# Kernel tuning notes

Measured on AMD Instinct MI355X. Metric: run time of the kernel, lower is better.

The kernel has to match this reference:

```python
import jax, jax.numpy as jnp
import numpy as np

NF, D, H = 32, 256, 128  # n_features, d_model, d_model//2
B, T = 16, 512
EPS = 1e-5

def _ln(x, g, b):
    m = jnp.mean(x, axis=-1, keepdims=True)
    v = jnp.mean((x - m) ** 2, axis=-1, keepdims=True)
    return (x - m) * jax.lax.rsqrt(v + EPS) * g + b


def setup_inputs() -> dict:
    key = jax.random.key(0)
    ks = jax.random.split(key, 16)
    s = 0.05
    inp = {
        "x": jax.random.normal(ks[0], (B, T, NF), dtype=jnp.float32),
        # batched per-feature GRN params (d_in=1 -> fc1 weight is (NF,H))
        "w1": jax.random.normal(ks[1], (NF, H)) * s,
        "b1": jnp.zeros((NF, H)),
        "w2": jax.random.normal(ks[2], (NF, H, D)) * s,
        "b2": jnp.zeros((NF, D)),
        "wg": jax.random.normal(ks[3], (NF, H, D)) * s,
        "bg": jnp.zeros((NF, D)),
        "ws": jax.random.normal(ks[4], (NF, D)) * s,  # skip Linear(1,D)
        "bs": jnp.zeros((NF, D)),
        "ln_g": jnp.ones((NF, D)),
        "ln_b": jnp.zeros((NF, D)),
        # weight GRN: d_in=NF*D, d_hidden=D, d_out=NF
        "W1": jax.random.normal(ks[5], (NF * D, D)) * s,
        "B1": jnp.zeros((D,)),
        "W2": jax.random.normal(ks[6], (D, NF)) * s,
        "B2": jnp.zeros((NF,)),
        "Wg": jax.random.normal(ks[7], (D, NF)) * s,
        "Bg": jnp.zeros((NF,)),
        "Ws": jax.random.normal(ks[8], (NF * D, NF)) * s,
        "Bs": jnp.zeros((NF,)),
        "LN_g": jnp.ones((NF,)),
        "LN_b": jnp.zeros((NF,)),
    }
    return inp


def reference(x, w1, b1, w2, b2, wg, bg, ws, bs, ln_g, ln_b,
              W1, B1, W2, B2, Wg, Bg, Ws, Bs, LN_g, LN_b):
    Bn, Tn, Fn = x.shape
    # --- all per-feature GRNs batched over the feature axis (dropout=eval/identity) ---
    h = jax.nn.elu(x[..., None] * w1 + b1)                      # (B,T,F,H)
    proj = jnp.einsum('btfh,fhd->btfd', h, w2) + b2             # (B,T,F,D)
    gate = jax.nn.sigmoid(jnp.einsum('btfh,fhd->btfd', h, wg) + bg)
    skip = x[..., None] * ws + bs                               # (B,T,F,D)
    stacked = _ln(skip + gate * proj, ln_g, ln_b)               # (B,T,F,D)
    # --- softmax feature weights from mean-pooled flat features ---
    flat_pooled = stacked.mean(axis=1).reshape(Bn, Fn * stacked.shape[-1])  # (B,F*D)
    hw = jax.nn.elu(flat_pooled @ W1 + B1)                      # (B,D)
    pw = hw @ W2 + B2
    gw = jax.nn.sigmoid(hw @ Wg + Bg)
    wgrn = _ln(flat_pooled @ Ws + Bs + gw * pw, LN_g, LN_b)     # (B,F)
    weights = jax.nn.softmax(wgrn, axis=-1)                     # (B,F)
    # --- weighted feature combine ---
    selected = jnp.einsum('btfd,bf->btd', stacked, weights)     # (B,T,D)
    return selected, weights
```

## Files before the change

### kernel.cpp

```cpp
#include <hip/hip_runtime.h>
#include <hip/hip_fp16.h>

#define NF 32
#define DM 256
#define HH 128
#define BB 16
#define TT 512
#define BT 8192
#define OUT_W_OFF 2097152
#define EPS 1e-5f

typedef __bf16 bf16x8 __attribute__((ext_vector_type(8)));
typedef float  f32x16 __attribute__((ext_vector_type(16)));
typedef __fp16 f16x2 __attribute__((ext_vector_type(2)));
typedef __fp16 f16x8 __attribute__((ext_vector_type(8)));

__device__ __forceinline__ float eluf(float z){ return z > 0.f ? z : __expf(z) - 1.f; }
__device__ __forceinline__ float sigm(float z){ return 1.f/(1.f + __expf(-z)); }
__device__ __forceinline__ unsigned f2bf(float x){
  unsigned u = __float_as_uint(x);
  u += 0x7fffu + ((u>>16)&1u);
  return u>>16;
}

template<int MT, int NTHR>
__device__ __forceinline__ void build_A(uint4* Apack, const float* __restrict__ x,
                                        const float* __restrict__ w1, const float* __restrict__ b1,
                                        int f, int tok0, int tid){
  #pragma unroll
  for (int p = 0; p < (MT*512)/NTHR; ++p){
    int slot = tid + p*NTHR;
    int l  = slot & 63;
    int ks = (slot>>6)&7;
    int mt = slot>>9;
    int m  = mt*32 + (l&31);
    int k0 = ks*16 + (l>>5)*8;
    float xv = x[(tok0+m)*NF + f];
    const float* wp = w1 + f*HH + k0;
    const float* bp = b1 + f*HH + k0;
    float4 wa = *(const float4*)wp, wb = *(const float4*)(wp+4);
    float4 ba = *(const float4*)bp, bb = *(const float4*)(bp+4);
    bf16x8 v;
    v[0] = (__bf16)eluf(fmaf(xv, wa.x, ba.x));
    v[1] = (__bf16)eluf(fmaf(xv, wa.y, ba.y));
    v[2] = (__bf16)eluf(fmaf(xv, wa.z, ba.z));
    v[3] = (__bf16)eluf(fmaf(xv, wa.w, ba.w));
    v[4] = (__bf16)eluf(fmaf(xv, wb.x, bb.x));
    v[5] = (__bf16)eluf(fmaf(xv, wb.y, bb.y));
    v[6] = (__bf16)eluf(fmaf(xv, wb.z, bb.z));
    v[7] = (__bf16)eluf(fmaf(xv, wb.w, bb.w));
    Apack[slot] = __builtin_bit_cast(uint4, v);
  }
}

__global__ __launch_bounds__(256) void k_prep(const float* __restrict__ w2,
                                              const float* __restrict__ wgm,
                                              uint4* __restrict__ Wpk,
                                              float* __restrict__ pooled,
                                              float* __restrict__ hw_pre,
                                              float* __restrict__ sk_pre,
                                              unsigned* __restrict__ counter){
  __shared__ float ssrc[2][128][32];
  const int tid = threadIdx.x;
  const int f = blockIdx.x, c = blockIdx.y;
  {
    const int gb = blockIdx.y*gridDim.x + blockIdx.x;
    const int gt = gb*256 + tid;
    pooled[gt] = 0.f;
    pooled[gt + 65536] = 0.f;
    if (gt < 4096) hw_pre[gt] = 0.f;
    else if (gt < 4608) sk_pre[gt - 4096] = 0.f;
    if (gt == 0) *counter = 0u;
  }
  #pragma unroll
  for (int it = 0; it < 32; ++it){
    int idx = tid + it*256;
    int arr = idx >> 12;
    int rem = idx & 4095;
    int k = rem >> 5, dd = rem & 31;
    const float* src = arr ? wgm : w2;
    ssrc[arr][k][dd] = src[(f*HH + k)*DM + c*32 + dd];
  }
  __syncthreads();
  #pragma unroll
  for (int p = 0; p < 4; ++p){
    int oc = tid + p*256;
    int nt = oc>>9, ks = (oc>>6)&7, l = oc&63;
    int k0 = ks*16 + (l>>5)*8, dd = l&31;
    float v[8];
    #pragma unroll
    for (int j=0;j<8;++j) v[j] = ssrc[nt][k0+j][dd];
    uint4 pk;
    pk.x = f2bf(v[0]) | (f2bf(v[1])<<16);
    pk.y = f2bf(v[2]) | (f2bf(v[3])<<16);
    pk.z = f2bf(v[4]) | (f2bf(v[5])<<16);
    pk.w = f2bf(v[6]) | (f2bf(v[7])<<16);
    Wpk[(f*8 + c)*1024 + oc] = pk;
  }
}

__global__ __launch_bounds__(512, 2) void k_pass1(const float* __restrict__ x,  const float* __restrict__ w1,
    const float* __restrict__ b1, const float* __restrict__ b2, const float* __restrict__ bg,
    const float* __restrict__ wsk, const float* __restrict__ bsk,
    const float* __restrict__ lng, const float* __restrict__ lnb,
    const uint4* __restrict__ Wpk,
    float* __restrict__ pooled, uint4* __restrict__ stk4){
  __shared__ uint4 smem[4096];
  __shared__ float xs[128];
  __shared__ float poolbuf[256];
  const int tid = threadIdx.x, lane = tid&63, wid = tid>>6;
  const int tt = wid>>1, ch = wid&1;
  const int col = lane&31, q = lane>>5;
  const int f = blockIdx.y;
  const int tok0 = blockIdx.x*128;
  const int b = tok0 >> 9;
  if (tid < 256) poolbuf[tid] = 0.f;
  if (tid < 128) xs[tid] = x[(tok0 + tid)*NF + f];

  build_A<4,512>(smem, x, w1, b1, f, tok0, tid);
  __syncthreads();
  bf16x8 afr[8];
  #pragma unroll
  for (int ks=0; ks<8; ++ks) afr[ks] = __builtin_bit_cast(bf16x8, smem[(tt*8+ks)*64 + lane]);
  __syncthreads();

  __fp16* stage = (__fp16*)smem;
  #pragma unroll 1
  for (int ci=0; ci<4; ++ci){
    const int c = ch*4 + ci;
    const uint4* wb = Wpk + (f*8 + c)*1024;
    bf16x8 bfr[8];
    #pragma unroll
    for (int ks=0;ks<8;++ks) bfr[ks] = __builtin_bit_cast(bf16x8, wb[ks*64 + lane]);
    f32x16 acc0 = {0.f};
    #pragma unroll
    for (int ks=0;ks<8;++ks) acc0 = __builtin_amdgcn_mfma_f32_32x32x16_bf16(afr[ks], bfr[ks], acc0, 0,0,0);
    __builtin_amdgcn_sched_barrier(0);
    #pragma unroll
    for (int ks=0;ks<8;++ks) bfr[ks] = __builtin_bit_cast(bf16x8, wb[512 + ks*64 + lane]);
    f32x16 acc1 = {0.f};
    #pragma unroll
    for (int ks=0;ks<8;++ks) acc1 = __builtin_amdgcn_mfma_f32_32x32x16_bf16(afr[ks], bfr[ks], acc1, 0,0,0);
    __builtin_amdgcn_sched_barrier(0);
    const int d = c*32 + col;
    const float b2v = b2[f*DM+d], bgv = bg[f*DM+d];
    #pragma unroll
    for (int i=0;i<8;++i){
      const int r0 = 2*i, r1 = r0+1;
      const int t0 = tt*32 + (r0&3) + 8*(i>>1) + 4*q;
      stage[ t0   *256 + d] = (__fp16)(sigm(acc1[r0]+bgv)*(acc0[r0]+b2v));
      stage[(t0+1)*256 + d] = (__fp16)(sigm(acc1[r1]+bgv)*(acc0[r1]+b2v));
    }
  }
  __syncthreads();

  const int oc = tid & 31;
  float4 ga = *(const float4*)(lng + f*DM + oc*8);
  float4 gb = *(const float4*)(lng + f*DM + oc*8 + 4);
  float4 la = *(const float4*)(lnb + f*DM + oc*8);
  float4 lb = *(const float4*)(lnb + f*DM + oc*8 + 4);
  float4 wa = *(const float4*)(wsk + f*DM + oc*8);
  float4 wbv = *(const float4*)(wsk + f*DM + oc*8 + 4);
  float4 sa = *(const float4*)(bsk + f*DM + oc*8);
  float4 sb = *(const float4*)(bsk + f*DM + oc*8 + 4);
  float gj[8] = {ga.x,ga.y,ga.z,ga.w,gb.x,gb.y,gb.z,gb.w};
  float bj[8] = {la.x,la.y,la.z,la.w,lb.x,lb.y,lb.z,lb.w};
  float wj[8] = {wa.x,wa.y,wa.z,wa.w,wbv.x,wbv.y,wbv.z,wbv.w};
  float cj[8] = {sa.x,sa.y,sa.z,sa.w,sb.x,sb.y,sb.z,sb.w};
  float ps[8];
  #pragma unroll
  for (int j=0;j<8;++j) ps[j]=0.f;
  #pragma unroll
  for (int p=0;p<8;++p){
    int slot = tid + p*512;
    int t = slot >> 5;
    uint4 v = smem[slot];
    f16x8 s8 = __builtin_bit_cast(f16x8, v);
    float xt = xs[t];
    float s[8];
    float ssum = 0.f, ssq = 0.f;
    #pragma unroll
    for (int j=0;j<8;++j){
      s[j] = fmaf(xt, wj[j], cj[j]) + (float)s8[j];
      ssum += s[j];
      ssq = fmaf(s[j], s[j], ssq);
    }
    ssum += __shfl_xor(ssum,1);  ssq += __shfl_xor(ssq,1);
    ssum += __shfl_xor(ssum,2);  ssq += __shfl_xor(ssq,2);
    ssum += __shfl_xor(ssum,4);  ssq += __shfl_xor(ssq,4);
    ssum += __shfl_xor(ssum,8);  ssq += __shfl_xor(ssq,8);
    ssum += __shfl_xor(ssum,16); ssq += __shfl_xor(ssq,16);
    float mu = ssum * (1.f/256.f);
    float var = fmaf(-mu, mu, ssq*(1.f/256.f));
    float rs = rsqrtf(fmaxf(var, 0.f) + EPS);
    float nmr = -mu*rs;
    float sh[8];
    #pragma unroll
    for (int j=0;j<8;++j){
      sh[j] = fmaf(fmaf(s[j], rs, nmr), gj[j], bj[j]);
      ps[j] += sh[j];
    }
    uint4 pk;
    pk.x = __builtin_bit_cast(unsigned, __builtin_amdgcn_cvt_pkrtz(sh[0], sh[1]));
    pk.y = __builtin_bit_cast(unsigned, __builtin_amdgcn_cvt_pkrtz(sh[2], sh[3]));
    pk.z = __builtin_bit_cast(unsigned, __builtin_amdgcn_cvt_pkrtz(sh[4], sh[5]));
    pk.w = __builtin_bit_cast(unsigned, __builtin_amdgcn_cvt_pkrtz(sh[6], sh[7]));
    const int tg = tok0 + t;
    stk4[(size_t)(tg>>2)*4096 + (size_t)f*128 + (size_t)(tg&3)*32 + oc] = pk;
  }
  #pragma unroll
  for (int j=0;j<8;++j) ps[j] += __shfl_xor(ps[j], 32);
  if (q == 0){
    #pragma unroll
    for (int j=0;j<8;++j) atomicAdd(&poolbuf[oc*8 + j], ps[j]);
  }
  __syncthreads();
  if (tid < 256) atomicAdd(&pooled[b*8192 + f*DM + tid], poolbuf[tid]);
}

__global__ __launch_bounds__(256) void k_pass2(const float* __restrict__ pooled,
    const float* __restrict__ W1, const float* __restrict__ Wsm,
    float* __restrict__ hw_pre, float* __restrict__ sk_pre,
    const float* __restrict__ B1, const float* __restrict__ W2, const float* __restrict__ B2,
    const float* __restrict__ Wg, const float* __restrict__ Bg, const float* __restrict__ Bs,
    const float* __restrict__ LNg, const float* __restrict__ LNb,
    unsigned* __restrict__ counter, float* __restrict__ out, float* __restrict__ wsel){
  __shared__ float fl[512];
  __shared__ float hwt[16][256];
  __shared__ int amLast;
  const int tid = threadIdx.x;
  const int b = blockIdx.x;
  const int k0 = blockIdx.y * 512;
  fl[tid]       = pooled[b*8192 + k0 + tid]       * (1.f/512.f);
  fl[tid+256]   = pooled[b*8192 + k0 + tid + 256] * (1.f/512.f);
  __syncthreads();
  float acc = 0.f;
  const float* wcol = W1 + (size_t)k0*DM + tid;
  #pragma unroll 4
  for (int i=0;i<512;++i) acc = fmaf(fl[i], wcol[(size_t)i*DM], acc);
  atomicAdd(&hw_pre[b*DM + tid], acc);
  const int colj = tid & 31, sub = tid >> 5;
  float acc2 = 0.f;
  const float* wscol = Wsm + (size_t)(k0 + sub*64)*NF + colj;
  const float* fls = fl + sub*64;
  #pragma unroll 4
  for (int i=0;i<64;++i) acc2 = fmaf(fls[i], wscol[(size_t)i*NF], acc2);
  atomicAdd(&sk_pre[b*NF + colj], acc2);

  __threadfence();
  __syncthreads();
  if (tid == 0){
    unsigned old = atomicAdd(counter, 1u);
    amLast = (old == 255u) ? 1 : 0;
  }
  __syncthreads();
  if (!amLast) return;
  #pragma unroll
  for (int p=0;p<16;++p){
    float v = atomicAdd(&hw_pre[p*DM + tid], 0.f);
    hwt[p][tid] = eluf(v + B1[tid]);
  }
  __syncthreads();
  const int j = tid & 31;
  const int bl = tid >> 5;
  #pragma unroll 1
  for (int pass=0; pass<2; ++pass){
    const int bb = bl + pass*8;
    float ap = B2[j], ag = Bg[j];
    #pragma unroll 4
    for (int i=0;i<256;++i){ float h = hwt[bb][i]; ap = fmaf(h, W2[i*NF+j], ap); ag = fmaf(h, Wg[i*NF+j], ag); }
    float gw = sigm(ag);
    float v = atomicAdd(&sk_pre[bb*NF + j], 0.f) + Bs[j] + gw*ap;
    float s1 = v;
    s1 += __shfl_xor(s1,1); s1 += __shfl_xor(s1,2); s1 += __shfl_xor(s1,4); s1 += __shfl_xor(s1,8); s1 += __shfl_xor(s1,16);
    float mean = s1*(1.f/32.f);
    float dv = v - mean;
    float s2 = dv*dv;
    s2 += __shfl_xor(s2,1); s2 += __shfl_xor(s2,2); s2 += __shfl_xor(s2,4); s2 += __shfl_xor(s2,8); s2 += __shfl_xor(s2,16);
    float wn = fmaf(dv * rsqrtf(s2*(1.f/32.f) + EPS), LNg[j], LNb[j]);
    float mx = wn;
    mx = fmaxf(mx, __shfl_xor(mx,1)); mx = fmaxf(mx, __shfl_xor(mx,2)); mx = fmaxf(mx, __shfl_xor(mx,4));
    mx = fmaxf(mx, __shfl_xor(mx,8)); mx = fmaxf(mx, __shfl_xor(mx,16));
    float e = __expf(wn - mx);
    float se = e;
    se += __shfl_xor(se,1); se += __shfl_xor(se,2); se += __shfl_xor(se,4); se += __shfl_xor(se,8); se += __shfl_xor(se,16);
    float wgt = e / se;
    out[OUT_W_OFF + bb*NF + j] = wgt;
    wsel[bb*NF + j] = wgt;
  }
}

__global__ __launch_bounds__(256) void k_comb(const uint4* __restrict__ stk4,
    const float* __restrict__ wsel, float* __restrict__ out){
  __shared__ float wloc[NF];
  const int tid = threadIdx.x, lane = tid&63;
  const int tc = blockIdx.x;
  const int ts = tid>>6;
  const int t = tc*4 + ts;
  const int b = t >> 9;
  if (tid < NF) wloc[tid] = wsel[b*NF + tid];
  __syncthreads();
  const int oc = lane&31, fh = lane>>5;
  float acc[8];
  #pragma unroll
  for (int j=0;j<8;++j) acc[j]=0.f;
  #pragma unroll
  for (int j=0;j<16;++j){
    int f = fh*16 + j;
    uint4 v = stk4[(size_t)tc*4096 + f*128 + ts*32 + oc];
    f16x8 hv = __builtin_bit_cast(f16x8, v);
    float wf = wloc[f];
    #pragma unroll
    for (int jj=0;jj<8;++jj) acc[jj] = fmaf(wf, (float)hv[jj], acc[jj]);
  }
  #pragma unroll
  for (int jj=0;jj<8;++jj) acc[jj] += __shfl_xor(acc[jj], 32);
  if (fh == 0){
    float4* o = (float4*)(out + (size_t)t*DM + oc*8);
    o[0] = make_float4(acc[0],acc[1],acc[2],acc[3]);
    o[1] = make_float4(acc[4],acc[5],acc[6],acc[7]);
  }
}

extern "C" void kernel_launch(void* const* d_in, const int* in_sizes, int n_in,
                              void* d_out, int out_size, void* d_ws, size_t ws_size,
                              hipStream_t stream) {
  const float* x   = (const float*)d_in[0];
  const float* w1  = (const float*)d_in[1];
  const float* b1  = (const float*)d_in[2];
  const float* w2  = (const float*)d_in[3];
  const float* b2  = (const float*)d_in[4];
  const float* wgm = (const float*)d_in[5];
  const float* bg  = (const float*)d_in[6];
  const float* wsk = (const float*)d_in[7];
  const float* bsk = (const float*)d_in[8];
  const float* lng = (const float*)d_in[9];
  const float* lnb = (const float*)d_in[10];
  const float* W1  = (const float*)d_in[11];
  const float* B1  = (const float*)d_in[12];
  const float* W2  = (const float*)d_in[13];
  const float* B2  = (const float*)d_in[14];
  const float* Wg  = (const float*)d_in[15];
  const float* Bg  = (const float*)d_in[16];
  const float* Wsm = (const float*)d_in[17];
  const float* Bs  = (const float*)d_in[18];
  const float* LNg = (const float*)d_in[19];
  const float* LNb = (const float*)d_in[20];
  float* out = (float*)d_out;

  char* ws = (char*)d_ws;
  uint4* Wpk      = (uint4*)ws;
  uint4* stk4     = (uint4*)(ws + 4194304);
  float* pooled   = (float*)(ws + 138412032);
  float* hw_pre   = (float*)(ws + 138936320);
  float* sk_pre   = (float*)(ws + 138952704);
  float* wsel     = (float*)(ws + 138954752);
  unsigned* cnt   = (unsigned*)(ws + 138956800);

  k_prep<<<dim3(32,8), 256, 0, stream>>>(w2, wgm, Wpk, pooled, hw_pre, sk_pre, cnt);
  k_pass1<<<dim3(64,32), 512, 0, stream>>>(x, w1, b1, b2, bg, wsk, bsk, lng, lnb,
                                           Wpk, pooled, stk4);
  k_pass2<<<dim3(16,16), 256, 0, stream>>>(pooled, W1, Wsm, hw_pre, sk_pre,
                                           B1, W2, B2, Wg, Bg, Bs, LNg, LNb,
                                           cnt, out, wsel);
  k_comb<<<2048, 256, 0, stream>>>(stk4, wsel, out);
}
```

Baseline: 325.7 us.

## Batch all 16 rows per W1 load in pass2 GEMV to reuse weights

The pass2 reduction is reorganized so that each block handles a 64-row slice of W1 for all 16 batch rows at once, instead of one batch row per block. Each W1 element is read once and reused across 16 accumulators, which cuts W1 global traffic by 16x. The grid shrinks from 256 blocks to 128, with the last-block counter threshold adjusted to match. In exchange the kernel has fewer blocks, more registers per thread, and more atomics per block.

After: 292.8 us. 1.11x faster.

```diff
diff --git a/kernel.cpp b/kernel.cpp
--- a/kernel.cpp
+++ b/kernel.cpp
@@ -225,33 +225,46 @@
     const float* __restrict__ Wg, const float* __restrict__ Bg, const float* __restrict__ Bs,
     const float* __restrict__ LNg, const float* __restrict__ LNb,
     unsigned* __restrict__ counter, float* __restrict__ out, float* __restrict__ wsel){
-  __shared__ float fl[512];
+  __shared__ float fl[16][64];
   __shared__ float hwt[16][256];
   __shared__ int amLast;
   const int tid = threadIdx.x;
-  const int b = blockIdx.x;
-  const int k0 = blockIdx.y * 512;
-  fl[tid]       = pooled[b*8192 + k0 + tid]       * (1.f/512.f);
-  fl[tid+256]   = pooled[b*8192 + k0 + tid + 256] * (1.f/512.f);
-  __syncthreads();
-  float acc = 0.f;
-  const float* wcol = W1 + (size_t)k0*DM + tid;
+  const int k0 = blockIdx.x * 64;
+  #pragma unroll
+  for (int p=0;p<4;++p){
+    int idx = tid + p*256;
+    int bb = idx >> 6, ii = idx & 63;
+    fl[bb][ii] = pooled[bb*8192 + k0 + ii] * (1.f/512.f);
+  }
+  __syncthreads();
+  float acc[16];
+  #pragma unroll
+  for (int b=0;b<16;++b) acc[b]=0.f;
+  const float* wp = W1 + (size_t)k0*DM + tid;
   #pragma unroll 4
-  for (int i=0;i<512;++i) acc = fmaf(fl[i], wcol[(size_t)i*DM], acc);
-  atomicAdd(&hw_pre[b*DM + tid], acc);
-  const int colj = tid & 31, sub = tid >> 5;
-  float acc2 = 0.f;
-  const float* wscol = Wsm + (size_t)(k0 + sub*64)*NF + colj;
-  const float* fls = fl + sub*64;
-  #pragma unroll 4
-  for (int i=0;i<64;++i) acc2 = fmaf(fls[i], wscol[(size_t)i*NF], acc2);
-  atomicAdd(&sk_pre[b*NF + colj], acc2);
+  for (int i=0;i<64;++i){
+    float w = wp[(size_t)i*DM];
+    #pragma unroll
+    for (int b=0;b<16;++b) acc[b] = fmaf(fl[b][i], w, acc[b]);
+  }
+  #pragma unroll
+  for (int b=0;b<16;++b) atomicAdd(&hw_pre[b*DM + tid], acc[b]);
+  const int colj = tid & 31, bh = tid >> 5;
+  const float* wsp = Wsm + (size_t)k0*NF + colj;
+  #pragma unroll 1
+  for (int pass=0; pass<2; ++pass){
+    const int bb = bh + pass*8;
+    float a2 = 0.f;
+    #pragma unroll 4
+    for (int i=0;i<64;++i) a2 = fmaf(fl[bb][i], wsp[(size_t)i*NF], a2);
+    atomicAdd(&sk_pre[bb*NF + colj], a2);
+  }
 
   __threadfence();
   __syncthreads();
   if (tid == 0){
     unsigned old = atomicAdd(counter, 1u);
-    amLast = (old == 255u) ? 1 : 0;
+    amLast = (old == 127u) ? 1 : 0;
   }
   __syncthreads();
   if (!amLast) return;
@@ -360,8 +373,8 @@
   k_prep<<<dim3(32,8), 256, 0, stream>>>(w2, wgm, Wpk, pooled, hw_pre, sk_pre, cnt);
   k_pass1<<<dim3(64,32), 512, 0, stream>>>(x, w1, b1, b2, bg, wsk, bsk, lng, lnb,
                                            Wpk, pooled, stk4);
-  k_pass2<<<dim3(16,16), 256, 0, stream>>>(pooled, W1, Wsm, hw_pre, sk_pre,
-                                           B1, W2, B2, Wg, Bg, Bs, LNg, LNb,
-                                           cnt, out, wsel);
+  k_pass2<<<dim3(128), 256, 0, stream>>>(pooled, W1, Wsm, hw_pre, sk_pre,
+                                         B1, W2, B2, Wg, Bg, Bs, LNg, LNb,
+                                         cnt, out, wsel);
   k_comb<<<2048, 256, 0, stream>>>(stk4, wsel, out);
 }
```
